# Optimization experiments

Measured on AMD Instinct MI355X. Metric: run time of the kernel, lower is better.

Reference implementation:

```python
import jax, jax.numpy as jnp
import numpy as np

B, T, D_MODEL, D_K = 4, 4096, 1024, 64

def setup_inputs() -> dict:
    key = jax.random.key(0)
    k1, k2, k3, k4, k5 = jax.random.split(key, 5)
    x = jax.random.normal(k1, (B, T, D_MODEL), dtype=jnp.float32)
    # rotary freqs_cis as (real, imag) pairs: unit-magnitude like real RoPE
    theta = 10000.0
    inv = 1.0 / (theta ** (jnp.arange(0, D_K, 2, dtype=jnp.float32) / D_K))  # [D_K//2]
    ang = jnp.arange(T, dtype=jnp.float32)[:, None] * inv[None, :]           # [T, D_K//2]
    freqs_cis = jnp.stack([jnp.cos(ang), jnp.sin(ang)], axis=-1)             # [T, D_K//2, 2]
    scale = 1.0 / np.sqrt(D_MODEL)
    Wq = jax.random.normal(k2, (D_MODEL, D_K), dtype=jnp.float32) * scale
    Wk = jax.random.normal(k3, (D_MODEL, D_K), dtype=jnp.float32) * scale
    Wv = jax.random.normal(k4, (D_MODEL, D_K), dtype=jnp.float32) * scale
    return {"x": x, "freqs_cis": freqs_cis, "Wq": Wq, "Wk": Wk, "Wv": Wv}

def _apply_rope(t, fr, fi):
    # t: [B,T,D_K]; fr/fi: [T, D_K//2]. Complex mult on (even, odd) pairs.
    tp = t.reshape(*t.shape[:-1], D_K // 2, 2)       # [B,T,P,2]
    tr, ti = tp[..., 0], tp[..., 1]
    or_ = tr * fr - ti * fi
    oi_ = tr * fi + ti * fr
    return jnp.stack([or_, oi_], axis=-1).reshape(*t.shape[:-1], D_K)

def reference(x, freqs_cis, Wq, Wk, Wv):
    q = x @ Wq                                       # [B,T,D_K]
    k = x @ Wk
    v = x @ Wv
    fr, fi = freqs_cis[..., 0], freqs_cis[..., 1]    # [T, D_K//2]
    q = _apply_rope(q, fr, fi)
    k = _apply_rope(k, fr, fi)
    wei = jnp.einsum('btd,bsd->bts', q, k) * (D_K ** -0.5)   # [B,T,T]
    causal = jnp.tril(jnp.ones((T, T), dtype=bool))
    wei = jnp.where(causal, wei, -jnp.inf)
    wei = jax.nn.softmax(wei, axis=-1)
    return jnp.einsum('bts,bsd->btd', wei, v)        # [B,T,D_K]
```

## Files before the change

### kernel.cpp

```cpp
#include <hip/hip_runtime.h>
#include <hip/hip_bf16.h>

#define BB 4
#define TT 4096
#define DM 1024
#define DK 64
#define NSPLIT 8

using f32x4  = __attribute__((ext_vector_type(4))) float;
using bf16x8 = __attribute__((ext_vector_type(8))) short;

__device__ __forceinline__ short f2bf(float f) {
    __hip_bfloat16 h = __float2bfloat16(f);
    return __builtin_bit_cast(short, h);
}
__device__ __forceinline__ float bf2f(short s) {
    unsigned int u = ((unsigned int)(unsigned short)s) << 16;
    return __builtin_bit_cast(float, u);
}

__global__ __launch_bounds__(256) void wt_kernel(const float* __restrict__ Wq,
                                                 const float* __restrict__ Wk,
                                                 const float* __restrict__ Wv,
                                                 short* __restrict__ Wt) {
    int idx = blockIdx.x * 256 + threadIdx.x;
    if (idx >= 192 * 1024) return;
    int n = idx >> 10;
    int m = idx & 1023;
    const float* W = (n < 64) ? Wq : (n < 128) ? Wk : Wv;
    int c = n & 63;
    Wt[idx] = f2bf(W[m * 64 + c]);
}

__global__ __launch_bounds__(256, 2) void proj_rope(const float* __restrict__ x,
                                                    const float* __restrict__ freqs,
                                                    const short* __restrict__ Wt,
                                                    short* __restrict__ q,
                                                    short* __restrict__ k,
                                                    short* __restrict__ vt)
{
    __shared__ short As[2][2048];
    __shared__ short Bs[2][12288];

    int t  = threadIdx.x;
    int w  = t >> 6;
    int l  = t & 63;
    int lr = l & 15;
    int lg = (l >> 4) & 3;
    int wr = w & 1;
    int wc = w >> 1;
    int bx = blockIdx.x;
    int mt = (bx & 7) * 64 + (bx >> 3);
    int m0 = mt * 32;

    int arow = t >> 3, au = t & 7;
    int aswz = arow & 7;
    const float* gA = x + (size_t)(m0 + arow) * DM + au * 8;

    const short* gBsw = Wt + (size_t)(t >> 3) * DM + (((t & 7) ^ ((t >> 3) & 7)) << 3);
    int wvsh = (t >> 6) * 512;

    f32x4 ar[2];

#define LOADA(c_) do { int kk = (c_) << 6;                      \
        ar[0] = *(const f32x4*)(gA + kk);                       \
        ar[1] = *(const f32x4*)(gA + kk + 4);                   \
    } while (0)

#define WRITEA(buf_) do {                                                      \
        bf16x8 a0_;                                                            \
        _Pragma("unroll")                                                      \
        for (int j_ = 0; j_ < 4; ++j_) {                                       \
            a0_[j_] = f2bf(ar[0][j_]); a0_[4 + j_] = f2bf(ar[1][j_]);          \
        }                                                                      \
        *(bf16x8*)&As[buf_][arow * 64 + ((au ^ aswz) << 3)] = a0_;             \
    } while (0)

#define ISSUEB(buf_, c_) do { int kk = (c_) << 6;                              \
        _Pragma("unroll")                                                      \
        for (int j_ = 0; j_ < 6; ++j_)                                         \
            __builtin_amdgcn_global_load_lds(                                  \
                (const __attribute__((address_space(1))) void*)(gBsw + (size_t)(j_ * 32) * DM + kk), \
                (__attribute__((address_space(3))) void*)&Bs[buf_][j_ * 2048 + wvsh], \
                16, 0, 0);                                                     \
    } while (0)

    f32x4 acc[6];
#pragma unroll
    for (int i = 0; i < 6; ++i) acc[i] = (f32x4){0.f, 0.f, 0.f, 0.f};

    int r7 = lr & 7;
    int amrow = (wr * 16 + lr) * 64;
    int cur = 0;

#define COMPUTE() do {                                                         \
        _Pragma("unroll")                                                      \
        for (int s_ = 0; s_ < 2; ++s_) {                                       \
            int u0_ = s_ * 4 + lg;                                             \
            bf16x8 af_ = *(const bf16x8*)&As[cur][amrow + ((u0_ ^ r7) << 3)];  \
            _Pragma("unroll")                                                  \
            for (int nh_ = 0; nh_ < 3; ++nh_)                                  \
                _Pragma("unroll")                                              \
                for (int ntl_ = 0; ntl_ < 2; ++ntl_) {                         \
                    int row_ = nh_ * 64 + (wc * 2 + ntl_) * 16 + lr;           \
                    bf16x8 bfr_ = *(const bf16x8*)&Bs[cur][row_ * 64 + ((u0_ ^ r7) << 3)]; \
                    acc[nh_ * 2 + ntl_] = __builtin_amdgcn_mfma_f32_16x16x32_bf16(af_, bfr_, acc[nh_ * 2 + ntl_], 0, 0, 0); \
                }                                                              \
        }                                                                      \
    } while (0)

    LOADA(0); WRITEA(0); LOADA(1);
    ISSUEB(0, 0);
    __syncthreads();

    for (int ch = 0; ch < 16; ++ch) {
        if (ch + 1 < 16) ISSUEB(cur ^ 1, ch + 1);
        COMPUTE();
        if (ch + 1 < 16) {
            WRITEA(cur ^ 1);
            if (ch + 2 < 16) LOADA(ch + 2);
            __syncthreads();
            cur ^= 1;
        }
    }
#undef LOADA
#undef WRITEA
#undef ISSUEB
#undef COMPUTE

#pragma unroll
    for (int nh = 0; nh < 2; ++nh) {
        short* dst = nh ? k : q;
        float postscale = nh ? 1.0f : 0.125f;
#pragma unroll
        for (int r = 0; r < 4; ++r) {
            int tg = m0 + wr * 16 + lg * 4 + r;
            int tt = tg & (TT - 1);
#pragma unroll
            for (int ntl = 0; ntl < 2; ++ntl) {
                int c = wc * 32 + ntl * 16 + lr;
                float e = acc[nh * 2 + ntl][r];
                float p = __shfl_xor(e, 1);
                float2 f = ((const float2*)freqs)[(size_t)tt * 32 + (c >> 1)];
                float sgn = (c & 1) ? f.y : -f.y;
                dst[(size_t)tg * DK + c] = f2bf((e * f.x + p * sgn) * postscale);
            }
        }
    }

    __syncthreads();
    short* vs = &As[0][0];
#pragma unroll
    for (int r = 0; r < 4; ++r)
#pragma unroll
        for (int ntl = 0; ntl < 2; ++ntl)
            vs[(wr * 16 + lg * 4 + r) * 64 + wc * 32 + ntl * 16 + lr] = f2bf(acc[4 + ntl][r]);
    __syncthreads();
    int b    = mt >> 7;
    int tt0  = (mt & 127) * 32;
    int c    = t >> 2;
    int tgrp = t & 3;
    bf16x8 v0;
#pragma unroll
    for (int j = 0; j < 8; ++j) v0[j] = vs[(tgrp * 8 + j) * 64 + c];
    *(bf16x8*)(vt + ((size_t)b * DK + c) * TT + tt0 + tgrp * 8) = v0;
}

__global__ __launch_bounds__(256, 4) void attn_kernel(const short* __restrict__ q,
                                                      const short* __restrict__ k,
                                                      const short* __restrict__ vt,
                                                      short* __restrict__ po,
                                                      float* __restrict__ ml)
{
    __shared__ short Kb[64][64];
    __shared__ short Vb[64][64];
    __shared__ short pbuf[4][16][72];

    int w  = threadIdx.x >> 6;
    int l  = threadIdx.x & 63;
    int lr = l & 15;
    int lg = l >> 4;
    int b  = blockIdx.y;
    int s  = blockIdx.z;
    int qt = 63 - blockIdx.x;
    int q0 = qt * 64;
    int qrow_wave = q0 + w * 16;

    const short* qB = q  + (size_t)b * TT * DK;
    const short* kB = k  + (size_t)b * TT * DK;
    const short* vB = vt + (size_t)b * DK * TT;

    bf16x8 qf0 = *(const bf16x8*)(qB + (size_t)(qrow_wave + lr) * DK + 8 * lg);
    bf16x8 qf1 = *(const bf16x8*)(qB + (size_t)(qrow_wave + lr) * DK + 32 + 8 * lg);

    f32x4 of[4];
#pragma unroll
    for (int i = 0; i < 4; ++i) of[i] = (f32x4){0.f, 0.f, 0.f, 0.f};
    float m[4], lsum[4];
#pragma unroll
    for (int r = 0; r < 4; ++r) { m[r] = -INFINITY; lsum[r] = 0.f; }

    int nt = (qt >= s) ? ((qt - s + NSPLIT) >> 3) : 0;

    int srow = threadIdx.x >> 2;
    int u0   = (threadIdx.x & 3) * 2;
    int p0s  = ((u0) ^ (srow & 7)) * 8;
    int p1s  = ((u0 + 1) ^ (srow & 7)) * 8;

    bf16x8 kr0, kr1, vr0, vr1;
    short* mypb = &pbuf[w][0][0];

#define ISSUE(tile_) do {                                                        \
        int kv0_ = (tile_) << 6;                                                 \
        const short* gk_ = kB + (size_t)(kv0_ + srow) * DK + (u0 * 8);           \
        const short* gv_ = vB + (size_t)srow * TT + kv0_ + (u0 * 8);             \
        kr0 = *(const bf16x8*)gk_; kr1 = *(const bf16x8*)(gk_ + 8);              \
        vr0 = *(const bf16x8*)gv_; vr1 = *(const bf16x8*)(gv_ + 8);              \
    } while (0)

#define WRITE() do {                                                             \
        *(bf16x8*)&Kb[srow][p0s] = kr0;                                         \
        *(bf16x8*)&Kb[srow][p1s] = kr1;                                         \
        *(bf16x8*)&Vb[srow][p0s] = vr0;                                         \
        *(bf16x8*)&Vb[srow][p1s] = vr1;                                         \
    } while (0)

    if (nt > 0) {
        ISSUE(s); WRITE();
        if (nt > 1) ISSUE(s + NSPLIT);
        __syncthreads();
        for (int i = 0; i < nt; ++i) {
            int kv0 = (s + i * NSPLIT) << 6;

            f32x4 sc[4];
#pragma unroll
            for (int c = 0; c < 4; ++c) sc[c] = (f32x4){0.f, 0.f, 0.f, 0.f};
#pragma unroll
            for (int c = 0; c < 4; ++c) {
                int row = c * 16 + lr;
                bf16x8 kf0 = *(const bf16x8*)&Kb[row][((lg) ^ (row & 7)) * 8];
                bf16x8 kf1 = *(const bf16x8*)&Kb[row][((4 + lg) ^ (row & 7)) * 8];
                sc[c] = __builtin_amdgcn_mfma_f32_16x16x32_bf16(qf0, kf0, sc[c], 0, 0, 0);
                sc[c] = __builtin_amdgcn_mfma_f32_16x16x32_bf16(qf1, kf1, sc[c], 0, 0, 0);
            }

            if (kv0 == q0) {
#pragma unroll
                for (int r = 0; r < 4; ++r) {
                    int qg = qrow_wave + lg * 4 + r;
#pragma unroll
                    for (int c = 0; c < 4; ++c)
                        sc[c][r] = (kv0 + c * 16 + lr <= qg) ? sc[c][r] : -INFINITY;
                }
            }

            float mx[4];
#pragma unroll
            for (int r = 0; r < 4; ++r)
                mx[r] = fmaxf(fmaxf(sc[0][r], sc[1][r]), fmaxf(sc[2][r], sc[3][r]));
            bool needA = (mx[0] > m[0] + 8.f) || (mx[1] > m[1] + 8.f) ||
                         (mx[2] > m[2] + 8.f) || (mx[3] > m[3] + 8.f);
            if (__any(needA)) {
#pragma unroll
                for (int r = 0; r < 4; ++r) {
                    float t2 = mx[r];
                    t2 = fmaxf(t2, __shfl_xor(t2, 1));
                    t2 = fmaxf(t2, __shfl_xor(t2, 2));
                    t2 = fmaxf(t2, __shfl_xor(t2, 4));
                    t2 = fmaxf(t2, __shfl_xor(t2, 8));
                    float mn = fmaxf(m[r], t2);
                    float alpha = __expf(m[r] - mn);
                    m[r] = mn;
                    lsum[r] *= alpha;
#pragma unroll
                    for (int dt = 0; dt < 4; ++dt) of[dt][r] *= alpha;
                }
            }
#pragma unroll
            for (int r = 0; r < 4; ++r) {
                float p0 = __expf(sc[0][r] - m[r]);
                float p1 = __expf(sc[1][r] - m[r]);
                float p2 = __expf(sc[2][r] - m[r]);
                float p3 = __expf(sc[3][r] - m[r]);
                lsum[r] += (p0 + p1) + (p2 + p3);
                int prow = (lg * 4 + r) * 72;
                mypb[prow + lr]      = f2bf(p0);
                mypb[prow + 16 + lr] = f2bf(p1);
                mypb[prow + 32 + lr] = f2bf(p2);
                mypb[prow + 48 + lr] = f2bf(p3);
            }

#pragma unroll
            for (int ks = 0; ks < 2; ++ks) {
                bf16x8 pa = *(const bf16x8*)(mypb + lr * 72 + ks * 32 + 8 * lg);
#pragma unroll
                for (int dt = 0; dt < 4; ++dt) {
                    int row = dt * 16 + lr;
                    bf16x8 vf = *(const bf16x8*)&Vb[row][((ks * 4 + lg) ^ (row & 7)) * 8];
                    of[dt] = __builtin_amdgcn_mfma_f32_16x16x32_bf16(pa, vf, of[dt], 0, 0, 0);
                }
            }

            if (i + 1 < nt) {
                __syncthreads();
                WRITE();
                if (i + 2 < nt) ISSUE(s + (i + 2) * NSPLIT);
                __syncthreads();
            }
        }
    }
#undef ISSUE
#undef WRITE

#pragma unroll
    for (int r = 0; r < 4; ++r) {
        float ps = lsum[r];
        ps += __shfl_xor(ps, 1);
        ps += __shfl_xor(ps, 2);
        ps += __shfl_xor(ps, 4);
        ps += __shfl_xor(ps, 8);
        lsum[r] = ps;
    }

    short* myo  = po + (((size_t)b * 64 + qt) * NSPLIT + s) * 4096;
    float* myml = ml + (((size_t)b * 64 + qt) * NSPLIT + s) * 128;
#pragma unroll
    for (int r = 0; r < 4; ++r) {
        int row = w * 16 + lg * 4 + r;
#pragma unroll
        for (int dt = 0; dt < 4; ++dt) myo[row * 64 + dt * 16 + lr] = f2bf(of[dt][r]);
        if (lr == 0) { myml[row] = m[r]; myml[64 + row] = lsum[r]; }
    }
}

__global__ __launch_bounds__(256) void merge_kernel(const short* __restrict__ po,
                                                    const float* __restrict__ ml,
                                                    float* __restrict__ out)
{
    int qt = blockIdx.x;
    int b  = blockIdx.y;
    int row = threadIdx.x >> 2;
    int cg  = threadIdx.x & 3;

    size_t mlbase = ((size_t)b * 64 + qt) * NSPLIT * 128;
    float mm[NSPLIT], llv[NSPLIT];
#pragma unroll
    for (int s = 0; s < NSPLIT; ++s) {
        mm[s]  = ml[mlbase + s * 128 + row];
        llv[s] = ml[mlbase + s * 128 + 64 + row];
    }
    float M = -INFINITY;
#pragma unroll
    for (int s = 0; s < NSPLIT; ++s) M = fmaxf(M, mm[s]);
    float e[NSPLIT], den = 0.f;
#pragma unroll
    for (int s = 0; s < NSPLIT; ++s) { e[s] = __expf(mm[s] - M); den += e[s] * llv[s]; }
    float inv = 1.0f / den;

    size_t pbase = ((size_t)b * 64 + qt) * NSPLIT * 4096;
#pragma unroll
    for (int jj = 0; jj < 2; ++jj) {
        int col = cg * 16 + jj * 8;
        float acc8[8];
#pragma unroll
        for (int e2 = 0; e2 < 8; ++e2) acc8[e2] = 0.f;
#pragma unroll
        for (int s = 0; s < NSPLIT; ++s) {
            bf16x8 v = *(const bf16x8*)(po + pbase + s * 4096 + row * 64 + col);
#pragma unroll
            for (int e2 = 0; e2 < 8; ++e2) acc8[e2] += e[s] * bf2f(v[e2]);
        }
        float* orow = out + ((size_t)b * TT + qt * 64 + row) * DK + col;
#pragma unroll
        for (int e2 = 0; e2 < 8; ++e2) orow[e2] = acc8[e2] * inv;
    }
}

extern "C" void kernel_launch(void* const* d_in, const int* in_sizes, int n_in,
                              void* d_out, int out_size, void* d_ws, size_t ws_size,
                              hipStream_t stream) {
    const float* x     = (const float*)d_in[0];
    const float* freqs = (const float*)d_in[1];
    const float* Wq    = (const float*)d_in[2];
    const float* Wk    = (const float*)d_in[3];
    const float* Wv    = (const float*)d_in[4];
    float* out = (float*)d_out;

    char* ws = (char*)d_ws;
    short* Wt  = (short*)ws;
    short* qb  = (short*)(ws + 393216);
    short* kb  = (short*)(ws + 2490368);
    short* vtb = (short*)(ws + 4587520);
    short* po  = (short*)(ws + 6684672);
    float* ml  = (float*)(ws + 23461888);

    hipLaunchKernelGGL(wt_kernel, dim3(768), dim3(256), 0, stream, Wq, Wk, Wv, Wt);
    hipLaunchKernelGGL(proj_rope, dim3(512), dim3(256), 0, stream, x, freqs, Wt, qb, kb, vtb);
    hipLaunchKernelGGL(attn_kernel, dim3(64, BB, NSPLIT), dim3(256), 0, stream, qb, kb, vtb, po, ml);
    hipLaunchKernelGGL(merge_kernel, dim3(64, BB), dim3(256), 0, stream, po, ml, out);
}
```

Measured before the change: 65.83 us.

## Stage weight tiles through registers with two-deep prefetch instead of direct LDS loads

```diff
diff --git a/kernel.cpp b/kernel.cpp
--- a/kernel.cpp
+++ b/kernel.cpp
@@ -55,34 +55,33 @@
 
     int arow = t >> 3, au = t & 7;
     int aswz = arow & 7;
-    const float* gA = x + (size_t)(m0 + arow) * DM + au * 8;
-
-    const short* gBsw = Wt + (size_t)(t >> 3) * DM + (((t & 7) ^ ((t >> 3) & 7)) << 3);
-    int wvsh = (t >> 6) * 512;
-
-    f32x4 ar[2];
+    int bswz = (t >> 3) & 7;
+    const float* gA = x  + (size_t)(m0 + arow) * DM + au * 8;
+    const short* gB = Wt + (size_t)(t >> 3) * DM + (t & 7) * 8;
+
+    f32x4 ar[2]; bf16x8 brA[6], brB[6];
 
 #define LOADA(c_) do { int kk = (c_) << 6;                      \
         ar[0] = *(const f32x4*)(gA + kk);                       \
         ar[1] = *(const f32x4*)(gA + kk + 4);                   \
     } while (0)
 
-#define WRITEA(buf_) do {                                                      \
+#define LOADB(dst_, c_) do { int kk = (c_) << 6;                               \
+        _Pragma("unroll")                                                      \
+        for (int j_ = 0; j_ < 6; ++j_)                                         \
+            dst_[j_] = *(const bf16x8*)(gB + (size_t)(j_ * 32) * DM + kk);     \
+    } while (0)
+
+#define WRITELDS(buf_, bsrc_) do {                                             \
         bf16x8 a0_;                                                            \
         _Pragma("unroll")                                                      \
         for (int j_ = 0; j_ < 4; ++j_) {                                       \
             a0_[j_] = f2bf(ar[0][j_]); a0_[4 + j_] = f2bf(ar[1][j_]);          \
         }                                                                      \
         *(bf16x8*)&As[buf_][arow * 64 + ((au ^ aswz) << 3)] = a0_;             \
-    } while (0)
-
-#define ISSUEB(buf_, c_) do { int kk = (c_) << 6;                              \
         _Pragma("unroll")                                                      \
         for (int j_ = 0; j_ < 6; ++j_)                                         \
-            __builtin_amdgcn_global_load_lds(                                  \
-                (const __attribute__((address_space(1))) void*)(gBsw + (size_t)(j_ * 32) * DM + kk), \
-                (__attribute__((address_space(3))) void*)&Bs[buf_][j_ * 2048 + wvsh], \
-                16, 0, 0);                                                     \
+            *(bf16x8*)&Bs[buf_][(j_ * 32 + (t >> 3)) * 64 + (((t & 7) ^ bswz) << 3)] = bsrc_[j_]; \
     } while (0)
 
     f32x4 acc[6];
@@ -109,23 +108,34 @@
         }                                                                      \
     } while (0)
 
-    LOADA(0); WRITEA(0); LOADA(1);
-    ISSUEB(0, 0);
+    LOADA(0); LOADB(brA, 0);
+    WRITELDS(0, brA);
+    LOADA(1); LOADB(brA, 1);
+    LOADB(brB, 2);
     __syncthreads();
 
-    for (int ch = 0; ch < 16; ++ch) {
-        if (ch + 1 < 16) ISSUEB(cur ^ 1, ch + 1);
+    for (int ch = 0; ch < 16; ch += 2) {
         COMPUTE();
         if (ch + 1 < 16) {
-            WRITEA(cur ^ 1);
+            WRITELDS(cur ^ 1, brA);
             if (ch + 2 < 16) LOADA(ch + 2);
+            if (ch + 3 < 16) LOADB(brA, ch + 3);
             __syncthreads();
             cur ^= 1;
+
+            COMPUTE();
+            if (ch + 2 < 16) {
+                WRITELDS(cur ^ 1, brB);
+                if (ch + 3 < 16) LOADA(ch + 3);
+                if (ch + 4 < 16) LOADB(brB, ch + 4);
+                __syncthreads();
+                cur ^= 1;
+            }
         }
     }
 #undef LOADA
-#undef WRITEA
-#undef ISSUEB
+#undef LOADB
+#undef WRITELDS
 #undef COMPUTE
 
 #pragma unroll
```

New measurement: 61.28 us. 1.07x faster.
